# Kernel tuning notes

Measured on AMD Instinct MI355X. Metric: run time of the kernel, lower is better.

The kernel has to match this reference:

```python
import jax, jax.numpy as jnp
import numpy as np

N_NODES = 50000
N_EDGES = 640000
D_IN = 128
D_HID = 128
D_OUT = 128


def setup_inputs() -> dict:
    key = jax.random.key(0)
    ks = jax.random.split(key, 8)
    x = jax.random.normal(ks[0], (N_NODES, D_IN), dtype=jnp.float32)
    edge_index = jax.random.randint(ks[1], (2, N_EDGES), 0, N_NODES, dtype=jnp.int64)
    s1 = 1.0 / np.sqrt(D_IN)
    s2 = 1.0 / np.sqrt(D_HID)
    W1_l = jax.random.uniform(ks[2], (D_IN, D_HID), jnp.float32, -s1, s1)
    W1_r = jax.random.uniform(ks[3], (D_IN, D_HID), jnp.float32, -s1, s1)
    b1 = jnp.zeros((D_HID,), jnp.float32)
    W2_l = jax.random.uniform(ks[4], (D_HID, D_OUT), jnp.float32, -s2, s2)
    W2_r = jax.random.uniform(ks[5], (D_HID, D_OUT), jnp.float32, -s2, s2)
    b2 = jnp.zeros((D_OUT,), jnp.float32)
    return {"x": x, "edge_index": edge_index,
            "W1_l": W1_l, "b1": b1, "W1_r": W1_r,
            "W2_l": W2_l, "b2": b2, "W2_r": W2_r}


def _sage_conv(x, src, dst, W_l, b_l, W_r, n_nodes):
    # mean-aggregate neighbor (source) features onto destinations
    agg = jax.ops.segment_sum(x[src], dst, num_segments=n_nodes)  # [N, d]
    cnt = jax.ops.segment_sum(jnp.ones((src.shape[0],), x.dtype), dst,
                              num_segments=n_nodes)  # [N]
    mean = agg / jnp.maximum(cnt, 1.0)[:, None]
    # PyG SAGEConv: lin_l(aggr) [with bias] + lin_r(x) [root weight, no bias]
    return mean @ W_l + b_l + x @ W_r


def reference(x, edge_index, W1_l, b1, W1_r, W2_l, b2, W2_r):
    src, dst = edge_index[0], edge_index[1]
    n = x.shape[0]
    h = _sage_conv(x, src, dst, W1_l, b1, W1_r, n)
    h = jax.nn.relu(h)
    h = _sage_conv(h, src, dst, W2_l, b2, W2_r, n)
    return h
```

## Files before the change

### kernel.cpp

```cpp
#include <hip/hip_runtime.h>

#define N_NODES 50000
#define N_EDGES 640000
#define D 128

#define SCAN_BLOCK 256
#define SCAN_NBLK ((N_NODES + SCAN_BLOCK - 1) / SCAN_BLOCK)

typedef __attribute__((ext_vector_type(8))) short bf16x8;
typedef __attribute__((ext_vector_type(4))) float f32x4;

__device__ __forceinline__ unsigned short f2bf(float f) {
    union { float f; unsigned u; } v; v.f = f;
    unsigned u = v.u;
    unsigned r = u + 0x7FFFu + ((u >> 16) & 1u);
    return (unsigned short)(r >> 16);
}
__device__ __forceinline__ float bf2f(unsigned short s) {
    union { unsigned u; float f; } v; v.u = ((unsigned)s) << 16; return v.f;
}

__global__ void deg_kernel(const int* __restrict__ dst, int* __restrict__ deg) {
    int e = blockIdx.x * blockDim.x + threadIdx.x;
    if (e < N_EDGES) atomicAdd(&deg[dst[e]], 1);
}

__global__ __launch_bounds__(SCAN_BLOCK) void scan_partial(const int* __restrict__ deg,
                                                           int* __restrict__ partial) {
    __shared__ int sm[SCAN_BLOCK];
    const int t = threadIdx.x;
    const int i = blockIdx.x * SCAN_BLOCK + t;
    sm[t] = (i < N_NODES) ? deg[i] : 0;
    __syncthreads();
#pragma unroll
    for (int off = SCAN_BLOCK / 2; off > 0; off >>= 1) {
        if (t < off) sm[t] += sm[t + off];
        __syncthreads();
    }
    if (t == 0) partial[blockIdx.x] = sm[0];
}

__global__ __launch_bounds__(SCAN_BLOCK) void scan_final2(const int* __restrict__ deg,
                                                          const int* __restrict__ partial,
                                                          int* __restrict__ row_off,
                                                          int* __restrict__ cursor) {
    __shared__ int sm[SCAN_BLOCK];
    const int t = threadIdx.x;
    const int b = blockIdx.x;

    int acc = 0;
    for (int i = t; i < b; i += SCAN_BLOCK) acc += partial[i];
    sm[t] = acc;
    __syncthreads();
#pragma unroll
    for (int off = SCAN_BLOCK / 2; off > 0; off >>= 1) {
        if (t < off) sm[t] += sm[t + off];
        __syncthreads();
    }
    const int boff = sm[0];
    __syncthreads();

    const int i = b * SCAN_BLOCK + t;
    int v = (i < N_NODES) ? deg[i] : 0;
    sm[t] = v;
    __syncthreads();
    int x = v;
#pragma unroll
    for (int off = 1; off < SCAN_BLOCK; off <<= 1) {
        int y = (t >= off) ? sm[t - off] : 0;
        __syncthreads();
        x += y;
        sm[t] = x;
        __syncthreads();
    }
    int excl = x - v + boff;
    if (i < N_NODES) {
        row_off[i] = excl;
        cursor[i] = excl;
    }
    if (b == SCAN_NBLK - 1 && t == SCAN_BLOCK - 1) row_off[N_NODES] = x + boff;
}

__global__ void fill_csr(const int* __restrict__ src, const int* __restrict__ dst,
                         int* __restrict__ cursor, int* __restrict__ csr_src) {
    int e = blockIdx.x * blockDim.x + threadIdx.x;
    if (e < N_EDGES) {
        int pos = atomicAdd(&cursor[dst[e]], 1);
        csr_src[pos] = src[e];
    }
}

__global__ void cvt_and_wt(const float* __restrict__ x,
                           const float* __restrict__ W1l, const float* __restrict__ W1r,
                           const float* __restrict__ W2l, const float* __restrict__ W2r,
                           unsigned short* __restrict__ x_bf,
                           unsigned short* __restrict__ Wt1,
                           unsigned short* __restrict__ Wt2,
                           int* __restrict__ deg) {
    const int b = blockIdx.x;
    const int t = threadIdx.x;
    if (b < 3125) {
        int i = b * 256 + t;
        float4 a = *reinterpret_cast<const float4*>(&x[(size_t)i * 8]);
        float4 c = *reinterpret_cast<const float4*>(&x[(size_t)i * 8 + 4]);
        bf16x8 o;
        o[0] = (short)f2bf(a.x); o[1] = (short)f2bf(a.y);
        o[2] = (short)f2bf(a.z); o[3] = (short)f2bf(a.w);
        o[4] = (short)f2bf(c.x); o[5] = (short)f2bf(c.y);
        o[6] = (short)f2bf(c.z); o[7] = (short)f2bf(c.w);
        *reinterpret_cast<bf16x8*>(&x_bf[(size_t)i * 8]) = o;
    } else if (b < 3381) {
        const bool second = (b >= 3125 + 128);
        const float* Wl = second ? W2l : W1l;
        const float* Wr = second ? W2r : W1r;
        unsigned short* Wt = second ? Wt2 : Wt1;
        int i = (b - (second ? 3253 : 3125)) * 256 + t;
        int c = i >> 8, k = i & 255;
        float v = (k < 128) ? Wl[k * 128 + c] : Wr[(k - 128) * 128 + c];
        Wt[c * 256 + k] = f2bf(v);
    } else {
        int i = (b - 3381) * 256 + t;
        if (i < N_NODES) deg[i] = 0;
    }
}

__global__ __launch_bounds__(256) void gather_bf16(const unsigned short* __restrict__ feat,
                                                   const int* __restrict__ row_off,
                                                   const int* __restrict__ csr_src,
                                                   unsigned short* __restrict__ mean) {
    int node = (blockIdx.x * 256 + threadIdx.x) >> 6;
    int l = threadIdx.x & 63;
    int grp = l >> 4;
    int c8 = (l & 15) * 8;
    int beg = row_off[node];
    int end = row_off[node + 1];

    float s[8] = {};
    int kb = beg + grp * 4;
    int idx[4];
#pragma unroll
    for (int j = 0; j < 4; ++j) {
        int k = kb + j;
        idx[j] = (kb < end) ? csr_src[k < end ? k : end - 1] : 0;
    }
    while (kb < end) {
        bf16x8 v[4];
#pragma unroll
        for (int j = 0; j < 4; ++j)
            v[j] = *reinterpret_cast<const bf16x8*>(&feat[(size_t)idx[j] * D + c8]);
        int kb_n = kb + 16;
        int idx_n[4];
#pragma unroll
        for (int j = 0; j < 4; ++j) {
            int k = kb_n + j;
            idx_n[j] = (kb_n < end) ? csr_src[k < end ? k : end - 1] : 0;
        }
#pragma unroll
        for (int j = 0; j < 4; ++j) {
            float m = (kb + j < end) ? 1.0f : 0.0f;
#pragma unroll
            for (int q = 0; q < 8; ++q) s[q] += m * bf2f((unsigned short)v[j][q]);
        }
        kb = kb_n;
#pragma unroll
        for (int j = 0; j < 4; ++j) idx[j] = idx_n[j];
    }
#pragma unroll
    for (int j = 0; j < 8; ++j) {
        float v = s[j];
        v += __shfl_xor(v, 16, 64);
        v += __shfl_xor(v, 32, 64);
        s[j] = v;
    }
    if (grp == 0) {
        float inv = 1.0f / fmaxf((float)(end - beg), 1.0f);
        bf16x8 o;
#pragma unroll
        for (int j = 0; j < 8; ++j) o[j] = (short)f2bf(s[j] * inv);
        *reinterpret_cast<bf16x8*>(&mean[(size_t)node * D + c8]) = o;
    }
}

template <bool RELU, bool OUTBF16>
__global__ __launch_bounds__(512) void sage_gemm_mfma(
    const unsigned short* __restrict__ Amean,
    const unsigned short* __restrict__ Aroot,
    const unsigned short* __restrict__ Wt,
    const float* __restrict__ bias,
    float* __restrict__ outf,
    unsigned short* __restrict__ outb)
{
    __shared__ bf16x8 ws[4096];
    const int t = threadIdx.x;
    const int w = t >> 6;
    const int l = t & 63;
    const int row0 = blockIdx.x * 128 + w * 16;

    int arow = row0 + (l & 15);
    if (arow >= N_NODES) arow = N_NODES - 1;
    const int k8 = (l >> 4) * 8;

    bf16x8 a[8];
#pragma unroll
    for (int kc = 0; kc < 8; ++kc) {
        const unsigned short* ap = (kc < 4)
            ? &Amean[(size_t)arow * D + kc * 32 + k8]
            : &Aroot[(size_t)arow * D + (kc - 4) * 32 + k8];
        a[kc] = *reinterpret_cast<const bf16x8*>(ap);
    }

#pragma unroll
    for (int i = 0; i < 8; ++i) {
        int g = i * 512 + t;
        int col = g >> 5;
        int chunk = g & 31;
        ws[col * 32 + (chunk ^ (col & 7))] =
            *reinterpret_cast<const bf16x8*>(&Wt[(size_t)g * 8]);
    }
    __syncthreads();

    f32x4 acc[8] = {};
    const int l15 = l & 15;
    const int kg = l >> 4;
    const int swz = l & 7;
#pragma unroll
    for (int kc = 0; kc < 8; ++kc) {
#pragma unroll
        for (int c = 0; c < 8; ++c) {
            bf16x8 bfr = ws[c * 512 + l15 * 32 + ((kc * 4 + kg) ^ swz)];
            acc[c] = __builtin_amdgcn_mfma_f32_16x16x32_bf16(a[kc], bfr, acc[c], 0, 0, 0);
        }
    }

    const int rbase = row0 + kg * 4;
#pragma unroll
    for (int c = 0; c < 8; ++c) {
        const int col = c * 16 + l15;
        const float b = bias[col];
#pragma unroll
        for (int i = 0; i < 4; ++i) {
            int r = rbase + i;
            if (r < N_NODES) {
                float v = acc[c][i] + b;
                if (RELU) v = fmaxf(v, 0.f);
                if (OUTBF16) outb[(size_t)r * D + col] = f2bf(v);
                else         outf[(size_t)r * D + col] = v;
            }
        }
    }
}

extern "C" void kernel_launch(void* const* d_in, const int* in_sizes, int n_in,
                              void* d_out, int out_size, void* d_ws, size_t ws_size,
                              hipStream_t stream) {
    const float* x   = (const float*)d_in[0];
    const int*   ei  = (const int*)d_in[1];
    const float* W1l = (const float*)d_in[2];
    const float* b1  = (const float*)d_in[3];
    const float* W1r = (const float*)d_in[4];
    const float* W2l = (const float*)d_in[5];
    const float* b2  = (const float*)d_in[6];
    const float* W2r = (const float*)d_in[7];
    float* out = (float*)d_out;

    const int* src = ei;
    const int* dst = ei + N_EDGES;

    int* deg       = (int*)d_ws;
    int* row_off   = deg + 51200;
    int* cursor    = row_off + 51200;
    int* partial   = cursor + 51200;
    int* pad       = partial + 256;
    int* csr_src   = pad + 256;
    unsigned short* x_bf    = (unsigned short*)(csr_src + N_EDGES);
    unsigned short* h_bf    = x_bf + (size_t)N_NODES * D;
    unsigned short* mean_bf = h_bf + (size_t)N_NODES * D;
    unsigned short* Wt1     = mean_bf + (size_t)N_NODES * D;
    unsigned short* Wt2     = Wt1 + 128 * 256;

    cvt_and_wt<<<3577, 256, 0, stream>>>(x, W1l, W1r, W2l, W2r, x_bf, Wt1, Wt2, deg);
    deg_kernel<<<(N_EDGES + 255) / 256, 256, 0, stream>>>(dst, deg);
    scan_partial<<<SCAN_NBLK, SCAN_BLOCK, 0, stream>>>(deg, partial);
    scan_final2<<<SCAN_NBLK, SCAN_BLOCK, 0, stream>>>(deg, partial, row_off, cursor);
    fill_csr<<<(N_EDGES + 255) / 256, 256, 0, stream>>>(src, dst, cursor, csr_src);

    const int gather_grid = N_NODES * 64 / 256;
    const int gemm_grid = (N_NODES + 127) / 128;

    gather_bf16<<<gather_grid, 256, 0, stream>>>(x_bf, row_off, csr_src, mean_bf);
    sage_gemm_mfma<true, true><<<gemm_grid, 512, 0, stream>>>(
        mean_bf, x_bf, Wt1, b1, nullptr, h_bf);

    gather_bf16<<<gather_grid, 256, 0, stream>>>(h_bf, row_off, csr_src, mean_bf);
    sage_gemm_mfma<false, false><<<gemm_grid, 512, 0, stream>>>(
        mean_bf, h_bf, Wt2, b2, out, nullptr);
}
```

Measured before the change: 154.4 us.

## Merge scan passes into one kernel and load GEMM weights directly to LDS

The two-pass prefix scan becomes a single kernel: each block sums every degree before its own range straight from the degree array instead of reading per-block partials, which drops one launch. This adds quadratic redundant reads of the degree array, up to 50K ints for the last blocks. Separately, the GEMM weight staging now uses global_load_lds to copy directly into shared memory, with the swizzle moved to the source address so the register round-trip is skipped.

Result: slower. 180.7 us (+17.0%).

```diff
diff --git a/kernel.cpp b/kernel.cpp
--- a/kernel.cpp
+++ b/kernel.cpp
@@ -25,31 +25,16 @@
     if (e < N_EDGES) atomicAdd(&deg[dst[e]], 1);
 }
 
-__global__ __launch_bounds__(SCAN_BLOCK) void scan_partial(const int* __restrict__ deg,
-                                                           int* __restrict__ partial) {
-    __shared__ int sm[SCAN_BLOCK];
-    const int t = threadIdx.x;
-    const int i = blockIdx.x * SCAN_BLOCK + t;
-    sm[t] = (i < N_NODES) ? deg[i] : 0;
-    __syncthreads();
-#pragma unroll
-    for (int off = SCAN_BLOCK / 2; off > 0; off >>= 1) {
-        if (t < off) sm[t] += sm[t + off];
-        __syncthreads();
-    }
-    if (t == 0) partial[blockIdx.x] = sm[0];
-}
-
-__global__ __launch_bounds__(SCAN_BLOCK) void scan_final2(const int* __restrict__ deg,
-                                                          const int* __restrict__ partial,
-                                                          int* __restrict__ row_off,
-                                                          int* __restrict__ cursor) {
+__global__ __launch_bounds__(SCAN_BLOCK) void scan_kernel2(const int* __restrict__ deg,
+                                                           int* __restrict__ row_off,
+                                                           int* __restrict__ cursor) {
     __shared__ int sm[SCAN_BLOCK];
     const int t = threadIdx.x;
     const int b = blockIdx.x;
 
     int acc = 0;
-    for (int i = t; i < b; i += SCAN_BLOCK) acc += partial[i];
+    const int limit = b * SCAN_BLOCK;
+    for (int i = t; i < limit; i += SCAN_BLOCK) acc += deg[i];
     sm[t] = acc;
     __syncthreads();
 #pragma unroll
@@ -211,11 +196,14 @@
 
 #pragma unroll
     for (int i = 0; i < 8; ++i) {
-        int g = i * 512 + t;
-        int col = g >> 5;
-        int chunk = g & 31;
-        ws[col * 32 + (chunk ^ (col & 7))] =
-            *reinterpret_cast<const bf16x8*>(&Wt[(size_t)g * 8]);
+        int s = i * 512 + t;
+        int col = s >> 5;
+        int chunk = s & 31;
+        int srcslot = col * 32 + (chunk ^ (col & 7));
+        __builtin_amdgcn_global_load_lds(
+            (const __attribute__((address_space(1))) unsigned int*)&Wt[(size_t)srcslot * 8],
+            (__attribute__((address_space(3))) unsigned int*)&ws[i * 512 + w * 64],
+            16, 0, 0);
     }
     __syncthreads();
 
@@ -269,9 +257,8 @@
     int* deg       = (int*)d_ws;
     int* row_off   = deg + 51200;
     int* cursor    = row_off + 51200;
-    int* partial   = cursor + 51200;
-    int* pad       = partial + 256;
-    int* csr_src   = pad + 256;
+    int* pad       = cursor + 51200;
+    int* csr_src   = pad + 512;
     unsigned short* x_bf    = (unsigned short*)(csr_src + N_EDGES);
     unsigned short* h_bf    = x_bf + (size_t)N_NODES * D;
     unsigned short* mean_bf = h_bf + (size_t)N_NODES * D;
@@ -280,8 +267,7 @@
 
     cvt_and_wt<<<3577, 256, 0, stream>>>(x, W1l, W1r, W2l, W2r, x_bf, Wt1, Wt2, deg);
     deg_kernel<<<(N_EDGES + 255) / 256, 256, 0, stream>>>(dst, deg);
-    scan_partial<<<SCAN_NBLK, SCAN_BLOCK, 0, stream>>>(deg, partial);
-    scan_final2<<<SCAN_NBLK, SCAN_BLOCK, 0, stream>>>(deg, partial, row_off, cursor);
+    scan_kernel2<<<SCAN_NBLK, SCAN_BLOCK, 0, stream>>>(deg, row_off, cursor);
     fill_csr<<<(N_EDGES + 255) / 256, 256, 0, stream>>>(src, dst, cursor, csr_src);
 
     const int gather_grid = N_NODES * 64 / 256;
```
